# Optimization experiments

Hardware: AMD Instinct MI355X
Metric: run time of the kernel (lower is better)

## Reference

```python
import jax, jax.numpy as jnp
import numpy as np

S, B, D, E, F = 2048, 2, 1024, 8, 4096


def setup_inputs() -> dict:
    key = jax.random.key(0)
    ks = jax.random.split(key, 6)
    x = jax.random.normal(ks[0], (S, B, D), dtype=jnp.float32)
    w_switch = jax.random.normal(ks[1], (D, E), dtype=jnp.float32) / np.sqrt(D)
    b_switch = jnp.zeros((E,), dtype=jnp.float32)
    w1 = jax.random.normal(ks[2], (E, D, F), dtype=jnp.float32) / np.sqrt(D)
    b1 = jnp.zeros((E, F), dtype=jnp.float32)
    w2 = jax.random.normal(ks[3], (E, F, D), dtype=jnp.float32) / np.sqrt(F)
    b2 = jnp.zeros((E, D), dtype=jnp.float32)
    return {"x": x, "w_switch": w_switch, "b_switch": b_switch,
            "w1": w1, "b1": b1, "w2": w2, "b2": b2}


def reference(x, w_switch, b_switch, w1, b1, w2, b2):
    # x: [S, B, D] -> tokens [N, D]
    s, b, d = x.shape
    n_experts = w1.shape[0]
    xf = x.reshape(-1, d)                                    # [N, D]
    route_prob = jax.nn.softmax(xf @ w_switch + b_switch, axis=-1)  # [N, E]
    route_prob_max = jnp.max(route_prob, axis=-1)            # [N]
    routes = jnp.argmax(route_prob, axis=-1)                 # [N] int
    # is_scale_prob=True: scale token by its routing probability before FFN
    xs = xf * route_prob_max[:, None]                        # [N, D]
    # Per-expert FFN evaluated densely (drop_tokens=False => every token kept),
    # then each token selects its routed expert's output.
    h = jax.nn.relu(jnp.einsum('nd,edf->enf', xs, w1) + b1[:, None, :])  # [E, N, F]
    y = jnp.einsum('enf,efd->end', h, w2) + b2[:, None, :]               # [E, N, D]
    n = xf.shape[0]
    out = y[routes, jnp.arange(n)]                           # [N, D]
    counts = jnp.zeros((n_experts,), dtype=jnp.float32).at[routes].add(1.0)
    n_dropped = jnp.zeros((), dtype=jnp.int32)               # drop_tokens=False
    return out.reshape(s, b, d), counts, route_prob.sum(0), n_dropped
```

## Files before the change

### kernel.cpp

```cpp
#include <hip/hip_runtime.h>
#include <hip/hip_bf16.h>

#define NTOK 4096
#define DDIM 1024
#define NEXP 8
#define FDIM 4096
#define MAXTILES 40

typedef __attribute__((ext_vector_type(4))) float f32x4;
typedef __attribute__((ext_vector_type(8))) short bf16x8;

#define GLDS(g, l) __builtin_amdgcn_global_load_lds( \
    (const __attribute__((address_space(1))) unsigned int*)(g), \
    (__attribute__((address_space(3))) unsigned int*)(l), 16, 0, 0)

__global__ __launch_bounds__(256) void route_kernel(
    const float* __restrict__ x,
    const float* __restrict__ w_switch,
    const float* __restrict__ b_switch,
    __hip_bfloat16* __restrict__ xs,
    int* __restrict__ amax_arr,
    float* __restrict__ partial)
{
    const int tid = threadIdx.x;
    const int wave = tid >> 6, lane = tid & 63;
    __shared__ float pr[4][16];

    float wacc[16];
#pragma unroll
    for (int j = 0; j < 16; j++) wacc[j] = 0.0f;

    for (int i = 0; i < 4; i++) {
        const int n = blockIdx.x * 16 + wave * 4 + i;
        const float4* xr = (const float4*)(x + (size_t)n * DDIM);
        float4 xv[4];
#pragma unroll
        for (int j = 0; j < 4; j++) xv[j] = xr[lane + j * 64];

        float acc[NEXP];
#pragma unroll
        for (int e = 0; e < NEXP; e++) acc[e] = 0.0f;
#pragma unroll
        for (int j = 0; j < 4; j++) {
            const int dbase = (lane + j * 64) * 4;
#pragma unroll
            for (int c = 0; c < 4; c++) {
                const float4* wr = (const float4*)(w_switch + (size_t)(dbase + c) * NEXP);
                float4 w0 = wr[0], w1 = wr[1];
                float xvc = ((const float*)&xv[j])[c];
                acc[0] += xvc * w0.x; acc[1] += xvc * w0.y;
                acc[2] += xvc * w0.z; acc[3] += xvc * w0.w;
                acc[4] += xvc * w1.x; acc[5] += xvc * w1.y;
                acc[6] += xvc * w1.z; acc[7] += xvc * w1.w;
            }
        }
#pragma unroll
        for (int e = 0; e < NEXP; e++) {
            float v = acc[e];
#pragma unroll
            for (int off = 32; off > 0; off >>= 1) v += __shfl_xor(v, off, 64);
            acc[e] = v;
        }
        float mx = -1e30f;
#pragma unroll
        for (int e = 0; e < NEXP; e++) {
            acc[e] += b_switch[e];
            mx = fmaxf(mx, acc[e]);
        }
        float sum = 0.0f;
#pragma unroll
        for (int e = 0; e < NEXP; e++) { acc[e] = __expf(acc[e] - mx); sum += acc[e]; }
        float inv = 1.0f / sum;
        float pmax = -1.0f; int amax = 0;
#pragma unroll
        for (int e = 0; e < NEXP; e++) {
            float p = acc[e] * inv;
            acc[e] = p;
            if (p > pmax) { pmax = p; amax = e; }
        }
#pragma unroll
        for (int e = 0; e < NEXP; e++) {
            wacc[e] += acc[e];
            wacc[8 + e] += (amax == e) ? 1.0f : 0.0f;
        }
        if (lane == 0) amax_arr[n] = amax;
#pragma unroll
        for (int j = 0; j < 4; j++) {
            ushort4 pk;
            __hip_bfloat16* pp = (__hip_bfloat16*)&pk;
            pp[0] = __float2bfloat16(xv[j].x * pmax);
            pp[1] = __float2bfloat16(xv[j].y * pmax);
            pp[2] = __float2bfloat16(xv[j].z * pmax);
            pp[3] = __float2bfloat16(xv[j].w * pmax);
            *(ushort4*)(xs + (size_t)n * DDIM + (lane + j * 64) * 4) = pk;
        }
    }
    if (lane == 0) {
#pragma unroll
        for (int j = 0; j < 16; j++) pr[wave][j] = wacc[j];
    }
    __syncthreads();
    if (tid < 16)
        partial[blockIdx.x * 16 + tid] = pr[0][tid] + pr[1][tid] + pr[2][tid] + pr[3][tid];
}

__global__ __launch_bounds__(1024) void bucket_finalize_kernel(
    const int* __restrict__ amax_arr, const float* __restrict__ partial,
    int* __restrict__ bucket, int* __restrict__ ecnt,
    float* __restrict__ out_tail, int* __restrict__ table)
{
    __shared__ int ctr[NEXP];
    __shared__ float red[16][16];
    if (threadIdx.x < NEXP) ctr[threadIdx.x] = 0;
    __syncthreads();
    const int lane = threadIdx.x & 63;
    for (int c = 0; c < NTOK; c += 1024) {
        int t = c + threadIdx.x;
        int a = amax_arr[t];
#pragma unroll
        for (int e = 0; e < NEXP; e++) {
            bool my = (a == e);
            unsigned long long mask = __ballot(my);
            int cnt = __popcll(mask);
            int base = 0;
            if (lane == 0 && cnt) base = atomicAdd(&ctr[e], cnt);
            base = __shfl(base, 0, 64);
            if (my) {
                int rank = __popcll(mask & ((1ull << lane) - 1ull));
                bucket[e * NTOK + base + rank] = t;
            }
        }
    }
    if (threadIdx.x < 256) {
        const int j = threadIdx.x & 15, g = threadIdx.x >> 4;
        float s = 0.0f;
        for (int k = 0; k < 16; k++) s += partial[(size_t)(g + k * 16) * 16 + j];
        red[g][j] = s;
    }
    __syncthreads();
    if (threadIdx.x < NEXP) ecnt[threadIdx.x] = ctr[threadIdx.x];
    if (threadIdx.x < 16) {
        float t2 = 0.0f;
        for (int k = 0; k < 16; k++) t2 += red[k][threadIdx.x];
        int dst = (threadIdx.x < 8) ? (8 + threadIdx.x) : (threadIdx.x - 8);
        out_tail[dst] = t2;
    }
    if (threadIdx.x == 16) out_tail[16] = 0.0f;
    if (threadIdx.x == 0) {
        int idx = 0;
        for (int e = 0; e < NEXP; e++) {
            int cnt2 = ctr[e];
            for (int m0 = 0; m0 < cnt2; m0 += 128) table[idx++] = (e << 16) | m0;
        }
        for (; idx < MAXTILES; idx++) table[idx] = -1;
    }
}

template <int MODE, int K, int NN, int KS, int NX>
__device__ __forceinline__ void gemm_body(
    const __hip_bfloat16* __restrict__ A,
    const float* __restrict__ W,
    const float* __restrict__ bias,
    const int* __restrict__ bucket,
    const int* __restrict__ ecnt,
    const int* __restrict__ table,
    void* __restrict__ Out)
{
    const int bid = blockIdx.x;
    const int xcd = bid & 7;
    const int q = bid >> 3;
    const int x = q % NX;
    const int yk = (q / NX) % (MAXTILES / 8);
    const int z = q / (NX * (MAXTILES / 8));
    const int y = xcd + 8 * yk;

    const int entry = table[y];
    if (entry < 0) return;
    const int e = entry >> 16;
    const int m0 = entry & 0xffff;
    const int cnt = ecnt[e];
    const int n0 = x * 128;
    const int kbase = (K / KS) * z;

    __shared__ __align__(16) __hip_bfloat16 Asm[128 * 64];
    __shared__ __align__(16) __hip_bfloat16 Bsm[128 * 64];
    __shared__ int toks[128];

    const int tid = threadIdx.x;
    if (tid < 128) {
        int r = m0 + tid;
        toks[tid] = bucket[e * NTOK + (r < cnt ? r : cnt - 1)];
    }
    __syncthreads();

    const int wave = tid >> 6, lane = tid & 63;

    const int srow = lane >> 3;
    const int swzcol = ((lane & 7) ^ srow) * 16;
    const char* pA[4];
#pragma unroll
    for (int i = 0; i < 4; i++)
        pA[i] = (const char*)(A + (size_t)toks[wave * 32 + i * 8 + srow] * K + kbase) + swzcol;

    const int ng = tid & 31;
    const int kg = tid >> 5;
    const float* pW = W + ((size_t)e * K + kbase + kg * 8) * NN + n0 + ng * 4;
    unsigned bofs[4];
#pragma unroll
    for (int c = 0; c < 4; c++) {
        const int n = ng * 4 + c;
        bofs[c] = n * 128 + ((kg ^ (n & 7)) * 16);
    }

    const int wm = wave & 1, wn = wave >> 1;
    const int r16 = lane & 15, kq16 = lane >> 4;
    const int r7x = (r16 & 7) * 16;

    f32x4 acc[4][4];
#pragma unroll
    for (int t = 0; t < 4; t++)
#pragma unroll
        for (int u = 0; u < 4; u++) acc[t][u] = (f32x4){0.f, 0.f, 0.f, 0.f};

    for (int k0 = 0; k0 < K / KS; k0 += 64) {
#pragma unroll
        for (int i = 0; i < 4; i++) {
            GLDS(pA[i], (char*)Asm + (wave * 32 + i * 8) * 128 + lane * 16);
            pA[i] += 128;
        }
        float4 v[8];
#pragma unroll
        for (int j = 0; j < 8; j++) v[j] = *(const float4*)(pW + (size_t)j * NN);
        pW += (size_t)64 * NN;
#pragma unroll
        for (int c = 0; c < 4; c++) {
            __hip_bfloat16 row[8];
#pragma unroll
            for (int j = 0; j < 8; j++)
                row[j] = __float2bfloat16(((const float*)&v[j])[c]);
            *(uint4*)((char*)Bsm + bofs[c]) = *(const uint4*)row;
        }
        __syncthreads();

#pragma unroll
        for (int ksub = 0; ksub < 2; ksub++) {
            const int slot = ((kq16 + ksub * 4) * 16) ^ r7x;
            bf16x8 a[4], b[4];
#pragma unroll
            for (int t = 0; t < 4; t++)
                a[t] = *(const bf16x8*)((const char*)Asm +
                        (wm * 64 + t * 16 + r16) * 128 + slot);
#pragma unroll
            for (int u = 0; u < 4; u++)
                b[u] = *(const bf16x8*)((const char*)Bsm +
                        (wn * 64 + u * 16 + r16) * 128 + slot);
#pragma unroll
            for (int t = 0; t < 4; t++)
#pragma unroll
                for (int u = 0; u < 4; u++)
                    acc[t][u] = __builtin_amdgcn_mfma_f32_16x16x32_bf16(a[t], b[u], acc[t][u], 0, 0, 0);
        }
        __syncthreads();
    }

    const int quad = lane >> 4, l15 = lane & 15;
    float bv[4];
#pragma unroll
    for (int u = 0; u < 4; u++) {
        if (MODE == 0)
            bv[u] = bias[(size_t)e * NN + n0 + wn * 64 + u * 16 + l15];
        else
            bv[u] = (z == 0) ? bias[(size_t)e * NN + n0 + wn * 64 + u * 16 + l15] : 0.0f;
    }
#pragma unroll
    for (int t = 0; t < 4; t++) {
#pragma unroll
        for (int rr = 0; rr < 4; rr++) {
            int row = wm * 64 + t * 16 + quad * 4 + rr;
            if (m0 + row < cnt) {
                int tok = toks[row];
#pragma unroll
                for (int u = 0; u < 4; u++) {
                    int col = n0 + wn * 64 + u * 16 + l15;
                    float vv = acc[t][u][rr] + bv[u];
                    if (MODE == 0) {
                        vv = fmaxf(vv, 0.0f);
                        ((__hip_bfloat16*)Out)[(size_t)tok * NN + col] = __float2bfloat16(vv);
                    } else {
                        unsafeAtomicAdd(&((float*)Out)[(size_t)tok * NN + col], vv);
                    }
                }
            }
        }
    }
}

__global__ __launch_bounds__(256, 4) void gemm_ffn1(
    const __hip_bfloat16* __restrict__ A, const float* __restrict__ W,
    const float* __restrict__ bias, const int* __restrict__ bucket,
    const int* __restrict__ ecnt, const int* __restrict__ table, void* __restrict__ Out)
{
    gemm_body<0, DDIM, FDIM, 1, FDIM / 128>(A, W, bias, bucket, ecnt, table, Out);
}

__global__ __launch_bounds__(256, 4) void gemm_ffn2(
    const __hip_bfloat16* __restrict__ A, const float* __restrict__ W,
    const float* __restrict__ bias, const int* __restrict__ bucket,
    const int* __restrict__ ecnt, const int* __restrict__ table, void* __restrict__ Out)
{
    gemm_body<1, FDIM, DDIM, 4, DDIM / 128>(A, W, bias, bucket, ecnt, table, Out);
}

extern "C" void kernel_launch(void* const* d_in, const int* in_sizes, int n_in,
                              void* d_out, int out_size, void* d_ws, size_t ws_size,
                              hipStream_t stream) {
    const float* x        = (const float*)d_in[0];
    const float* w_switch = (const float*)d_in[1];
    const float* b_switch = (const float*)d_in[2];
    const float* w1       = (const float*)d_in[3];
    const float* b1       = (const float*)d_in[4];
    const float* w2       = (const float*)d_in[5];
    const float* b2       = (const float*)d_in[6];

    float* out = (float*)d_out;
    float* out_tail = out + (size_t)NTOK * DDIM;

    char* ws = (char*)d_ws;
    __hip_bfloat16* xs = (__hip_bfloat16*)(ws);
    __hip_bfloat16* h  = (__hip_bfloat16*)(ws + 8388608ull);
    int* bucket        = (int*)(ws + 109051904ull);
    int* amax_arr      = (int*)(ws + 109182976ull);
    float* partial     = (float*)(ws + 109199360ull);
    int* ecnt          = (int*)(ws + 109215744ull);
    int* table         = (int*)(ws + 109215776ull);

    hipMemsetAsync(out, 0, (size_t)NTOK * DDIM * sizeof(float), stream);

    hipLaunchKernelGGL(route_kernel, dim3(256), dim3(256), 0, stream,
                       x, w_switch, b_switch, xs, amax_arr, partial);
    hipLaunchKernelGGL(bucket_finalize_kernel, dim3(1), dim3(1024), 0, stream,
                       amax_arr, partial, bucket, ecnt, out_tail, table);

    hipLaunchKernelGGL(gemm_ffn1, dim3((FDIM / 128) * MAXTILES), dim3(256), 0, stream,
                       xs, w1, b1, bucket, ecnt, table, (void*)h);

    hipLaunchKernelGGL(gemm_ffn2, dim3((DDIM / 128) * MAXTILES * 4), dim3(256), 0, stream,
                       h, w2, b2, bucket, ecnt, table, (void*)out);
}
```

Baseline: 518.3 us.

## Pre-convert expert weights to bf16 and split waves into A/B loaders

Result: slower. 559.5 us (+8.0%).

```diff
diff --git a/kernel.cpp b/kernel.cpp
--- a/kernel.cpp
+++ b/kernel.cpp
@@ -156,10 +156,29 @@
     }
 }
 
+__global__ __launch_bounds__(256) void convert_kernel(
+    const float* __restrict__ in, __hip_bfloat16* __restrict__ outp)
+{
+    const size_t tg = (size_t)blockIdx.x * 256 + threadIdx.x;
+    const size_t stride = (size_t)2048 * 256;
+#pragma unroll
+    for (int it = 0; it < 8; ++it) {
+        const size_t i = (tg + (size_t)it * stride) * 8;
+        float4 a = *(const float4*)(in + i);
+        float4 b = *(const float4*)(in + i + 4);
+        __hip_bfloat16 r[8];
+        r[0] = __float2bfloat16(a.x); r[1] = __float2bfloat16(a.y);
+        r[2] = __float2bfloat16(a.z); r[3] = __float2bfloat16(a.w);
+        r[4] = __float2bfloat16(b.x); r[5] = __float2bfloat16(b.y);
+        r[6] = __float2bfloat16(b.z); r[7] = __float2bfloat16(b.w);
+        *(uint4*)(outp + i) = *(const uint4*)r;
+    }
+}
+
 template <int MODE, int K, int NN, int KS, int NX>
 __device__ __forceinline__ void gemm_body(
     const __hip_bfloat16* __restrict__ A,
-    const float* __restrict__ W,
+    const __hip_bfloat16* __restrict__ Wb,
     const float* __restrict__ bias,
     const int* __restrict__ bucket,
     const int* __restrict__ ecnt,
@@ -194,28 +213,31 @@
     __syncthreads();
 
     const int wave = tid >> 6, lane = tid & 63;
-
-    const int srow = lane >> 3;
-    const int swzcol = ((lane & 7) ^ srow) * 16;
-    const char* pA[4];
-#pragma unroll
-    for (int i = 0; i < 4; i++)
-        pA[i] = (const char*)(A + (size_t)toks[wave * 32 + i * 8 + srow] * K + kbase) + swzcol;
-
-    const int ng = tid & 31;
-    const int kg = tid >> 5;
-    const float* pW = W + ((size_t)e * K + kbase + kg * 8) * NN + n0 + ng * 4;
-    unsigned bofs[4];
-#pragma unroll
-    for (int c = 0; c < 4; c++) {
-        const int n = ng * 4 + c;
-        bofs[c] = n * 128 + ((kg ^ (n & 7)) * 16);
-    }
-
     const int wm = wave & 1, wn = wave >> 1;
     const int r16 = lane & 15, kq16 = lane >> 4;
     const int r7x = (r16 & 7) * 16;
 
+    const char* pA[8] = {};
+    const __hip_bfloat16* pW = nullptr;
+    unsigned bofs[8] = {};
+
+    if (wave < 2) {
+        const int srow = lane >> 3;
+        const int swzcol = ((lane & 7) ^ srow) * 16;
+#pragma unroll
+        for (int i = 0; i < 8; i++)
+            pA[i] = (const char*)(A + (size_t)toks[wave * 64 + i * 8 + srow] * K + kbase) + swzcol;
+    } else {
+        const int t2 = tid - 128;
+        const int n8 = t2 >> 3, k8 = t2 & 7;
+        pW = Wb + ((size_t)e * K + kbase + k8 * 8) * NN + n0 + n8 * 8;
+#pragma unroll
+        for (int c = 0; c < 8; c++) {
+            const int n = n8 * 8 + c;
+            bofs[c] = n * 128 + ((k8 ^ c) * 16);
+        }
+    }
+
     f32x4 acc[4][4];
 #pragma unroll
     for (int t = 0; t < 4; t++)
@@ -223,22 +245,27 @@
         for (int u = 0; u < 4; u++) acc[t][u] = (f32x4){0.f, 0.f, 0.f, 0.f};
 
     for (int k0 = 0; k0 < K / KS; k0 += 64) {
-#pragma unroll
-        for (int i = 0; i < 4; i++) {
-            GLDS(pA[i], (char*)Asm + (wave * 32 + i * 8) * 128 + lane * 16);
-            pA[i] += 128;
-        }
-        float4 v[8];
-#pragma unroll
-        for (int j = 0; j < 8; j++) v[j] = *(const float4*)(pW + (size_t)j * NN);
-        pW += (size_t)64 * NN;
-#pragma unroll
-        for (int c = 0; c < 4; c++) {
-            __hip_bfloat16 row[8];
+        if (wave < 2) {
+#pragma unroll
+            for (int i = 0; i < 8; i++) {
+                GLDS(pA[i], (char*)Asm + (wave * 64 + i * 8) * 128 + lane * 16);
+                pA[i] += 128;
+            }
+        } else {
+            unsigned v[8][4];
 #pragma unroll
             for (int j = 0; j < 8; j++)
-                row[j] = __float2bfloat16(((const float*)&v[j])[c]);
-            *(uint4*)((char*)Bsm + bofs[c]) = *(const uint4*)row;
+                *(uint4*)v[j] = *(const uint4*)(pW + (size_t)j * NN);
+            pW += (size_t)64 * NN;
+#pragma unroll
+            for (int c = 0; c < 8; c++) {
+                const unsigned sel = (c & 1) ? 0x07060302u : 0x05040100u;
+                unsigned o[4];
+#pragma unroll
+                for (int w = 0; w < 4; w++)
+                    o[w] = __builtin_amdgcn_perm(v[2 * w + 1][c >> 1], v[2 * w][c >> 1], sel);
+                *(uint4*)((char*)Bsm + bofs[c]) = *(const uint4*)o;
+            }
         }
         __syncthreads();
 
@@ -296,19 +323,19 @@
 }
 
 __global__ __launch_bounds__(256, 4) void gemm_ffn1(
-    const __hip_bfloat16* __restrict__ A, const float* __restrict__ W,
+    const __hip_bfloat16* __restrict__ A, const __hip_bfloat16* __restrict__ Wb,
     const float* __restrict__ bias, const int* __restrict__ bucket,
     const int* __restrict__ ecnt, const int* __restrict__ table, void* __restrict__ Out)
 {
-    gemm_body<0, DDIM, FDIM, 1, FDIM / 128>(A, W, bias, bucket, ecnt, table, Out);
+    gemm_body<0, DDIM, FDIM, 1, FDIM / 128>(A, Wb, bias, bucket, ecnt, table, Out);
 }
 
 __global__ __launch_bounds__(256, 4) void gemm_ffn2(
-    const __hip_bfloat16* __restrict__ A, const float* __restrict__ W,
+    const __hip_bfloat16* __restrict__ A, const __hip_bfloat16* __restrict__ Wb,
     const float* __restrict__ bias, const int* __restrict__ bucket,
     const int* __restrict__ ecnt, const int* __restrict__ table, void* __restrict__ Out)
 {
-    gemm_body<1, FDIM, DDIM, 4, DDIM / 128>(A, W, bias, bucket, ecnt, table, Out);
+    gemm_body<1, FDIM, DDIM, 4, DDIM / 128>(A, Wb, bias, bucket, ecnt, table, Out);
 }
 
 extern "C" void kernel_launch(void* const* d_in, const int* in_sizes, int n_in,
@@ -328,6 +355,7 @@
     char* ws = (char*)d_ws;
     __hip_bfloat16* xs = (__hip_bfloat16*)(ws);
     __hip_bfloat16* h  = (__hip_bfloat16*)(ws + 8388608ull);
+    __hip_bfloat16* wt = (__hip_bfloat16*)(ws + 41943040ull);
     int* bucket        = (int*)(ws + 109051904ull);
     int* amax_arr      = (int*)(ws + 109182976ull);
     float* partial     = (float*)(ws + 109199360ull);
@@ -341,9 +369,11 @@
     hipLaunchKernelGGL(bucket_finalize_kernel, dim3(1), dim3(1024), 0, stream,
                        amax_arr, partial, bucket, ecnt, out_tail, table);
 
+    hipLaunchKernelGGL(convert_kernel, dim3(2048), dim3(256), 0, stream, w1, wt);
     hipLaunchKernelGGL(gemm_ffn1, dim3((FDIM / 128) * MAXTILES), dim3(256), 0, stream,
-                       xs, w1, b1, bucket, ecnt, table, (void*)h);
-
+                       xs, wt, b1, bucket, ecnt, table, (void*)h);
+
+    hipLaunchKernelGGL(convert_kernel, dim3(2048), dim3(256), 0, stream, w2, wt);
     hipLaunchKernelGGL(gemm_ffn2, dim3((DDIM / 128) * MAXTILES * 4), dim3(256), 0, stream,
-                       h, w2, b2, bucket, ecnt, table, (void*)out);
-}
+                       h, wt, b2, bucket, ecnt, table, (void*)out);
+}
```
